# Optimization experiments

Hardware: AMD Instinct MI355X
Metric: run time of the kernel (lower is better)

The kernel has to match this reference:

```python
import jax, jax.numpy as jnp
import numpy as np

E = 512   # embed_dim == decoder_dim (structurally required by the module)
D = 512
V = 10000
B = 64
S = 32    # encoded caption length; max decode steps T = S - 1


def _lstm_cell(x, h, c, wih, whh, bih, bhh):
    # torch.nn.LSTMCell gate order: i, f, g, o
    gates = x @ wih.T + h @ whh.T + bih + bhh
    i, f, g, o = jnp.split(gates, 4, axis=-1)
    c2 = jax.nn.sigmoid(f) * c + jax.nn.sigmoid(i) * jnp.tanh(g)
    h2 = jax.nn.sigmoid(o) * jnp.tanh(c2)
    return h2, c2


def setup_inputs() -> dict:
    key = jax.random.key(0)
    ks = jax.random.split(key, 16)
    encoder_out = jax.random.normal(ks[0], (B, E), jnp.float32)
    encoded_captions = jax.random.randint(ks[1], (B, S), 0, V)
    # lengths sorted descending (required by the ragged :batch_size_t slicing); force max = S
    lens = np.sort(np.asarray(jax.random.randint(ks[2], (B,), 8, S + 1)))[::-1].copy()
    lens[0] = S
    caption_lengths = jnp.asarray(lens, jnp.int32)
    u = lambda k, sh: jax.random.uniform(k, sh, jnp.float32, -0.1, 0.1)
    return {
        'encoder_out': encoder_out,
        'encoded_captions': encoded_captions,
        'caption_lengths': caption_lengths,
        'embedding': u(ks[3], (V, E)),
        'dec_wih': u(ks[4], (4 * D, 2 * E)),
        'dec_whh': u(ks[5], (4 * D, D)),
        'dec_bih': u(ks[6], (4 * D,)),
        'dec_bhh': u(ks[7], (4 * D,)),
        'w_wih': u(ks[8], (4, E)),
        'w_whh': u(ks[9], (4, 1)),
        'w_bih': u(ks[10], (4,)),
        'w_bhh': u(ks[11], (4,)),
        'init_h_w': u(ks[12], (1, E)),
        'init_h_b': jnp.zeros((1,), jnp.float32),
        'init_c_w': u(ks[13], (1, E)),
        'init_c_b': jnp.zeros((1,), jnp.float32),
        'cls_w': u(ks[14], (V, D)),
        'cls_b': jnp.zeros((V,), jnp.float32),
    }


def reference(encoder_out, encoded_captions, caption_lengths, embedding,
              dec_wih, dec_whh, dec_bih, dec_bhh,
              w_wih, w_whh, w_bih, w_bhh,
              init_h_w, init_h_b, init_c_w, init_c_b,
              cls_w, cls_b):
    dl = caption_lengths - 1                      # decode lengths, [B]
    T = int(np.max(np.asarray(dl)))
    emb = embedding[encoded_captions]             # [B,S,E]
    xs = jnp.moveaxis(emb[:, :T, :], 1, 0)        # [T,B,E]
    wh0 = encoder_out @ init_h_w.T + init_h_b     # [B,1]
    wc0 = encoder_out @ init_c_w.T + init_c_b     # [B,1]

    def step(carry, inp):
        t, x_e = inp
        h, c, wh, wc = carry
        m = (dl > t).astype(x_e.dtype)[:, None]   # [B,1] active-row mask (ragged batch)
        wh2, wc2 = _lstm_cell(encoder_out, wh, wc, w_wih, w_whh, w_bih, w_bhh)
        x = jnp.concatenate([x_e, encoder_out], axis=-1)           # [B,2E]
        h2, c2 = _lstm_cell(x, h, c, dec_wih, dec_whh, dec_bih, dec_bhh)
        preds = (h2 @ cls_w.T + cls_b) * m        # inactive rows stay 0 (dropout is eval-mode identity)
        wgt = jax.nn.sigmoid(wh2)[:, 0] * m[:, 0] # [B]
        keep = m > 0
        carry = (jnp.where(keep, h2, h), jnp.where(keep, c2, c),
                 jnp.where(keep, wh2, wh), jnp.where(keep, wc2, wc))
        return carry, (preds, wgt)

    carry0 = (encoder_out, encoder_out, wh0, wc0)
    _, (p_seq, w_seq) = jax.lax.scan(step, carry0, (jnp.arange(T), xs))
    predictions = jnp.moveaxis(p_seq, 0, 1)                        # [B,T,V]
    weights = jnp.broadcast_to(w_seq.T[:, :, None], (B, T, V))     # replicate per-step scalar across vocab
    return predictions, dl, weights
```

## Files before the change

kernel.cpp:

```cpp
#include <hip/hip_runtime.h>
#include <hip/hip_bf16.h>


typedef __attribute__((ext_vector_type(4))) float f32x4;
typedef __attribute__((ext_vector_type(8))) short short8;
typedef __attribute__((ext_vector_type(4))) unsigned short u16x4;

#define BB 64
#define SS 32
#define TT 31
#define EE 512
#define VV 10000

__device__ __forceinline__ float sigf(float x){ return 1.0f/(1.0f + __expf(-x)); }
__device__ __forceinline__ float tanh_(float x){
  x = fminf(15.f, fmaxf(-15.f, x));
  float e = __expf(2.f*x);
  return (e-1.f)/(e+1.f);
}
__device__ __forceinline__ unsigned short f2bf(float x){
  __hip_bfloat16 h = __float2bfloat16(x);
  return __builtin_bit_cast(unsigned short, h);
}
__device__ __forceinline__ short8 cvt8(f32x4 a, f32x4 b){
  short8 t;
  t[0] = (short)f2bf(a.x); t[1] = (short)f2bf(a.y);
  t[2] = (short)f2bf(a.z); t[3] = (short)f2bf(a.w);
  t[4] = (short)f2bf(b.x); t[5] = (short)f2bf(b.y);
  t[6] = (short)f2bf(b.z); t[7] = (short)f2bf(b.w);
  return t;
}
__device__ __forceinline__ short8 ld16_coh(const void* p){
  short8 r;
  asm volatile("global_load_dwordx4 %0, %1, off sc0 sc1" : "=v"(r) : "v"(p) : "memory");
  return r;
}
__device__ __forceinline__ void st8_coh(void* p, unsigned long long v){
  asm volatile("global_store_dwordx2 %0, %1, off sc0 sc1" :: "v"(p), "v"(v) : "memory");
}

#define NPREP 2048
__global__ __launch_bounds__(256) void k_prep(
    const float* __restrict__ dwih, const float* __restrict__ dwhh,
    const float* __restrict__ emb, const int* __restrict__ cap,
    const float* __restrict__ enc,
    __hip_bfloat16* __restrict__ wihbf, __hip_bfloat16* __restrict__ whhbf,
    __hip_bfloat16* __restrict__ xa, __hip_bfloat16* __restrict__ h0,
    const int* __restrict__ caplen,
    const float* __restrict__ wwih, const float* __restrict__ wwhh,
    const float* __restrict__ wbih, const float* __restrict__ wbhh,
    const float* __restrict__ ihw, const float* __restrict__ ihb,
    const float* __restrict__ icw, const float* __restrict__ icb,
    float* __restrict__ wgt, unsigned* __restrict__ flags,
    float* __restrict__ dl_out)
{
  if (blockIdx.x >= NPREP){
    int b = blockIdx.x - NPREP;
    int w = threadIdx.x >> 6, lane = threadIdx.x & 63;
    __shared__ float sv[6];

    float p = 0.f;
    for (int k = lane; k < EE; k += 64) p += enc[b*EE + k] * wwih[w*EE + k];
    #pragma unroll
    for (int off = 32; off; off >>= 1) p += __shfl_down(p, off, 64);
    if (lane == 0) sv[w] = p;

    if (w < 2){
      const float* iw = (w == 0) ? ihw : icw;
      float q = 0.f;
      for (int k = lane; k < EE; k += 64) q += enc[b*EE + k] * iw[k];
      #pragma unroll
      for (int off = 32; off; off >>= 1) q += __shfl_down(q, off, 64);
      if (lane == 0) sv[4 + w] = q + ((w == 0) ? ihb[0] : icb[0]);
    }
    __syncthreads();

    if (threadIdx.x == 0){
      float wh = sv[4], wc = sv[5];
      int dl = caplen[b] - 1;
      for (int t = 0; t < TT; t++){
        float gi = sv[0] + wh*wwhh[0] + wbih[0] + wbhh[0];
        float gf = sv[1] + wh*wwhh[1] + wbih[1] + wbhh[1];
        float gg = sv[2] + wh*wwhh[2] + wbih[2] + wbhh[2];
        float go = sv[3] + wh*wwhh[3] + wbih[3] + wbhh[3];
        float wc2 = sigf(gf)*wc + sigf(gi)*tanh_(gg);
        float wh2 = sigf(go)*tanh_(wc2);
        float m = (dl > t) ? 1.f : 0.f;
        wgt[b*TT + t] = sigf(wh2) * m;
        if (dl > t){ wh = wh2; wc = wc2; }
      }
      dl_out[b] = (float)dl;
    }
    if (b == 0) for (int i = threadIdx.x; i < 4096; i += 256) flags[i] = 0;
    return;
  }

  const int n1 = 262144;
  const int n2 = n1 + 131072;
  const int n3 = n2 + 253952;
  const int n4 = n3 + 4096;
  for (int i = blockIdx.x*blockDim.x + threadIdx.x; i < n4; i += NPREP*256){
    const float* src; __hip_bfloat16* dst;
    if (i < n1){ src = dwih + (size_t)i*8; dst = wihbf + (size_t)i*8; }
    else if (i < n2){ int j = i - n1; src = dwhh + (size_t)j*8; dst = whhbf + (size_t)j*8; }
    else if (i < n3){
      int j = i - n2; int e = j*8;
      int r = e >> 10, k = e & 1023, t = r >> 6, b = r & 63;
      src = (k < 512) ? emb + (size_t)cap[b*SS + t]*EE + k
                      : enc + (size_t)b*EE + (k - 512);
      dst = xa + (size_t)e;
    } else {
      int j = i - n3; int e = j*8;
      src = enc + (size_t)e; dst = h0 + (size_t)e;
    }
    f32x4 lo = *(const f32x4*)src;
    f32x4 hi = *(const f32x4*)(src + 4);
    *(short8*)dst = cvt8(lo, hi);
  }
}

__global__ __launch_bounds__(256) void k_xproj(
    const __hip_bfloat16* __restrict__ xa, const __hip_bfloat16* __restrict__ wihbf,
    const float* __restrict__ bih, const float* __restrict__ bhh,
    float* __restrict__ xp)
{
  int bm = blockIdx.y;
  int bn = blockIdx.x;
  int w = threadIdx.x >> 6, lane = threadIdx.x & 63;
  int col = lane & 15, kg = lane >> 4;
  int m0 = bm*64;
  int n0 = bn*256 + w*64;

  f32x4 acc[4][4] = {};
  for (int kk = 0; kk < 32; kk++){
    short8 aW[4], aX[4];
    #pragma unroll
    for (int i = 0; i < 4; i++){
      aW[i] = *(const short8*)(wihbf + (size_t)(n0 + i*16 + col)*1024 + kk*32 + kg*8);
      aX[i] = *(const short8*)(xa    + (size_t)(m0 + i*16 + col)*1024 + kk*32 + kg*8);
    }
    #pragma unroll
    for (int nt = 0; nt < 4; nt++)
      #pragma unroll
      for (int mt = 0; mt < 4; mt++)
        acc[nt][mt] = __builtin_amdgcn_mfma_f32_16x16x32_bf16(aW[nt], aX[mt], acc[nt][mt], 0, 0, 0);
  }
  #pragma unroll
  for (int nt = 0; nt < 4; nt++){
    int n = n0 + nt*16 + 4*kg;
    f32x4 badd = *(const f32x4*)(bih + n);
    f32x4 b2   = *(const f32x4*)(bhh + n);
    badd = badd + b2;
    #pragma unroll
    for (int mt = 0; mt < 4; mt++){
      int r = m0 + mt*16 + col;
      *(f32x4*)(xp + (size_t)r*2048 + n) = acc[nt][mt] + badd;
    }
  }
}

__global__ __launch_bounds__(64, 1) void k_rec(
    const __hip_bfloat16* __restrict__ whhbf,
    const float* __restrict__ xp,
    const float* __restrict__ enc,
    const int* __restrict__ caplen,
    char* __restrict__ hbuf,
    __hip_bfloat16* __restrict__ hout,
    unsigned* __restrict__ flags,
    const float* __restrict__ clsw,
    __hip_bfloat16* __restrict__ clsbf)
{
  const int bid = blockIdx.x;
  const int lane = threadIdx.x;

  if (bid >= 128){
    const int n4 = 1280000;
    for (int i = (bid - 128)*64 + lane; i < n4; i += 384*64){
      f32x4 v = ((const f32x4*)clsw)[i];
      u16x4 o;
      o.x = f2bf(v.x); o.y = f2bf(v.y); o.z = f2bf(v.z); o.w = f2bf(v.w);
      ((u16x4*)clsbf)[i] = o;
    }
    return;
  }

  const int g = bid >> 5, s = bid & 31;
  const int col = lane & 15, kg = lane >> 4;
  const int d0 = s*16;
  const int b  = g*16 + col;
  const int dbase = d0 + 4*kg;
  const int pme = (dbase >> 2);

  short8 Aq[4][16];
  #pragma unroll
  for (int q = 0; q < 4; q++){
    const __hip_bfloat16* wrow = whhbf + (size_t)(q*512 + d0 + col)*512;
    #pragma unroll
    for (int kk = 0; kk < 16; kk++)
      Aq[q][kk] = *(const short8*)(wrow + kk*32 + kg*8);
  }
  #pragma unroll
  for (int q = 0; q < 4; q++)
    #pragma unroll
    for (int kk = 0; kk < 16; kk++)
      asm volatile("" : "+v"(Aq[q][kk]));

  float hst[4], cst[4];
  #pragma unroll
  for (int j = 0; j < 4; j++){
    float e0 = enc[(size_t)b*EE + dbase + j];
    hst[j] = e0; cst[j] = e0;
  }
  const int dl = caplen[b] - 1;
  unsigned* myflag = flags + (size_t)(g*32 + s)*32;
  const unsigned* pollflag = flags + (size_t)(g*32 + (lane & 31))*32;

  f32x4 xg[4];
  #pragma unroll
  for (int q = 0; q < 4; q++)
    xg[q] = *(const f32x4*)(xp + (size_t)b*2048 + q*512 + dbase);

  for (int t = 0; t < TT; t++){
    if (t > 0){
      const unsigned tgt = (unsigned)t;
      while (1){
        unsigned v = __hip_atomic_load(pollflag, __ATOMIC_RELAXED, __HIP_MEMORY_SCOPE_AGENT);
        v = min(v, (unsigned)__shfl_xor((int)v, 1, 64));
        v = min(v, (unsigned)__shfl_xor((int)v, 2, 64));
        v = min(v, (unsigned)__shfl_xor((int)v, 4, 64));
        v = min(v, (unsigned)__shfl_xor((int)v, 8, 64));
        v = min(v, (unsigned)__shfl_xor((int)v, 16, 64));
        if (v >= tgt) break;
        __builtin_amdgcn_s_sleep(1);
      }
    }

    const char* hc = hbuf + (size_t)(t & 1)*65536 + (size_t)b*1024 + kg*16;
    short8 Bf[16];
    #pragma unroll
    for (int kk = 0; kk < 16; kk++)
      Bf[kk] = ld16_coh(hc + kk*64);

    f32x4 xgn[4];
    if (t + 1 < TT){
      #pragma unroll
      for (int q = 0; q < 4; q++)
        xgn[q] = *(const f32x4*)(xp + (size_t)((t+1)*BB + b)*2048 + q*512 + dbase);
    }

    asm volatile("s_waitcnt vmcnt(0)" ::: "memory");
    __builtin_amdgcn_sched_barrier(0);

    f32x4 acc[4] = {};
    #pragma unroll
    for (int kk = 0; kk < 16; kk++)
      #pragma unroll
      for (int q = 0; q < 4; q++)
        acc[q] = __builtin_amdgcn_mfma_f32_16x16x32_bf16(Aq[q][kk], Bf[kk], acc[q], 0, 0, 0);

    const bool act = dl > t;
    unsigned long long hpack = 0, spack = 0;
    #pragma unroll
    for (int j = 0; j < 4; j++){
      float gi = acc[0][j] + xg[0][j];
      float gf = acc[1][j] + xg[1][j];
      float gg = acc[2][j] + xg[2][j];
      float go = acc[3][j] + xg[3][j];
      float c2 = sigf(gf)*cst[j] + sigf(gi)*tanh_(gg);
      float h2 = sigf(go)*tanh_(c2);
      if (act){ cst[j] = c2; hst[j] = h2; }
      hpack |= (unsigned long long)f2bf(h2)     << (16*j);
      spack |= (unsigned long long)f2bf(hst[j]) << (16*j);
    }

    ((unsigned long long*)hout)[((size_t)b*TT + t)*128 + pme] = hpack;

    if (t < TT - 1){
      st8_coh(hbuf + (size_t)((t + 1) & 1)*65536 + (size_t)b*1024 + (size_t)dbase*2, spack);
      asm volatile("s_waitcnt vmcnt(0)" ::: "memory");
      if (lane == 0)
        __hip_atomic_store(myflag, (unsigned)(t + 1),
                           __ATOMIC_RELAXED, __HIP_MEMORY_SCOPE_AGENT);
    }

    #pragma unroll
    for (int q = 0; q < 4; q++) xg[q] = xgn[q];
  }
}

__global__ __launch_bounds__(256) void k_cls(
    const __hip_bfloat16* __restrict__ hbf,
    const __hip_bfloat16* __restrict__ wbf,
    const float* __restrict__ clsb,
    const float* __restrict__ wgt,
    float* __restrict__ preds, float* __restrict__ wout)
{
  int bid = blockIdx.x;
  int bn = bid % 79, bm = bid / 79;
  int w = threadIdx.x >> 6, lane = threadIdx.x & 63;
  int col = lane & 15, kg = lane >> 4;
  int r0 = bm*128 + (w >> 1)*64;
  int v0 = bn*128 + (w & 1)*64;
  if (r0 >= 1984) return;

  int vrow[4], rrow[4];
  #pragma unroll
  for (int i = 0; i < 4; i++){
    vrow[i] = min(v0 + i*16 + col, VV - 1);
    rrow[i] = min(r0 + i*16 + col, 1983);
  }
  f32x4 acc[4][4] = {};
  for (int kk = 0; kk < 16; kk++){
    short8 a[4], b[4];
    #pragma unroll
    for (int i = 0; i < 4; i++){
      a[i] = *(const short8*)(wbf + (size_t)vrow[i]*512 + kk*32 + kg*8);
      b[i] = *(const short8*)(hbf + (size_t)rrow[i]*512 + kk*32 + kg*8);
    }
    #pragma unroll
    for (int vt = 0; vt < 4; vt++)
      #pragma unroll
      for (int rt = 0; rt < 4; rt++)
        acc[vt][rt] = __builtin_amdgcn_mfma_f32_16x16x32_bf16(a[vt], b[rt], acc[vt][rt], 0, 0, 0);
  }

  #pragma unroll
  for (int vt = 0; vt < 4; vt++){
    int v = v0 + vt*16 + 4*kg;
    if (v >= VV) continue;
    f32x4 cb4 = *(const f32x4*)(clsb + v);
    #pragma unroll
    for (int rt = 0; rt < 4; rt++){
      int r = r0 + rt*16 + col;
      if (r >= 1984) continue;
      float wv = wgt[r];
      float mf = (wv > 0.f) ? 1.f : 0.f;
      f32x4 o = (acc[vt][rt] + cb4) * mf;
      f32x4 wq = {wv, wv, wv, wv};
      *(f32x4*)(preds + (size_t)r*VV + v) = o;
      *(f32x4*)(wout  + (size_t)r*VV + v) = wq;
    }
  }
}

extern "C" void kernel_launch(void* const* d_in, const int* in_sizes, int n_in,
                              void* d_out, int out_size, void* d_ws, size_t ws_size,
                              hipStream_t stream) {
  const float* enc    = (const float*)d_in[0];
  const int*   cap    = (const int*)  d_in[1];
  const int*   caplen = (const int*)  d_in[2];
  const float* emb    = (const float*)d_in[3];
  const float* dwih   = (const float*)d_in[4];
  const float* dwhh   = (const float*)d_in[5];
  const float* dbih   = (const float*)d_in[6];
  const float* dbhh   = (const float*)d_in[7];
  const float* wwih   = (const float*)d_in[8];
  const float* wwhh   = (const float*)d_in[9];
  const float* wbih   = (const float*)d_in[10];
  const float* wbhh   = (const float*)d_in[11];
  const float* ihw    = (const float*)d_in[12];
  const float* ihb    = (const float*)d_in[13];
  const float* icw    = (const float*)d_in[14];
  const float* icb    = (const float*)d_in[15];
  const float* clsw   = (const float*)d_in[16];
  const float* clsb   = (const float*)d_in[17];

  float* preds  = (float*)d_out;
  float* dl_out = preds + (size_t)BB*TT*VV;
  float* wout   = dl_out + BB;

  char* ws = (char*)d_ws;
  float*          wgt   = (float*)         (ws + 0);
  unsigned*       flags = (unsigned*)      (ws + 8192);
  __hip_bfloat16* clsbf = (__hip_bfloat16*)(ws + 24576);
  __hip_bfloat16* wihbf = (__hip_bfloat16*)(ws + 10264576);
  __hip_bfloat16* whhbf = (__hip_bfloat16*)(ws + 14458880);
  __hip_bfloat16* xa    = (__hip_bfloat16*)(ws + 16556032);
  float*          xp    = (float*)         (ws + 20619264);
  char*           hbuf  = (char*)          (ws + 36872192);
  __hip_bfloat16* hout  = (__hip_bfloat16*)(ws + 37003264);

  k_prep <<<NPREP + BB, 256, 0, stream>>>(dwih, dwhh, emb, cap, enc,
                                          wihbf, whhbf, xa,
                                          (__hip_bfloat16*)hbuf,
                                          caplen, wwih, wwhh, wbih, wbhh,
                                          ihw, ihb, icw, icb, wgt, flags, dl_out);
  k_xproj<<<dim3(8, 31), 256, 0, stream>>>(xa, wihbf, dbih, dbhh, xp);
  k_rec  <<<512, 64, 0, stream>>>(whhbf, xp, enc, caplen, hbuf, hout, flags,
                                  clsw, clsbf);
  k_cls  <<<16*79, 256, 0, stream>>>(hout, clsbf, clsb, wgt, preds, wout);
}
```

Before: 292.3 us.

## Swap MFMA operand roles in classifier and split weights broadcast into separate blocks

The classifier GEMM now puts hidden rows in the A operand and vocab rows in B. Each lane therefore holds four consecutive rows for one vocab column, and lanes 0-15 write consecutive columns, so the scalar preds stores coalesce along the vocab dimension. The weights output broadcast moves out of the GEMM epilogue into 1984 extra row-blocks that stream vectorized float4 stores. This takes the strided 16-byte stores of the old layout off the GEMM tiles, at the cost of scalar 4-byte stores for preds and more blocks.

```diff
diff --git a/kernel.cpp b/kernel.cpp
--- a/kernel.cpp
+++ b/kernel.cpp
@@ -296,51 +296,65 @@
     float* __restrict__ preds, float* __restrict__ wout)
 {
   int bid = blockIdx.x;
+  if (bid >= 1264){
+    int r = bid - 1264;
+    float wv = wgt[r];
+    f32x4 wq = {wv, wv, wv, wv};
+    f32x4* dst = (f32x4*)(wout + (size_t)r*VV);
+    #pragma unroll 2
+    for (int i = threadIdx.x; i < VV/4; i += 256)
+      dst[i] = wq;
+    return;
+  }
+
   int bn = bid % 79, bm = bid / 79;
   int w = threadIdx.x >> 6, lane = threadIdx.x & 63;
   int col = lane & 15, kg = lane >> 4;
-  int r0 = bm*128 + (w >> 1)*64;
-  int v0 = bn*128 + (w & 1)*64;
-  if (r0 >= 1984) return;
-
-  int vrow[4], rrow[4];
+  int m0 = bm*128 + (w >> 1)*64;
+  int n0 = bn*128 + (w & 1)*64;
+  if (m0 >= 1984) return;
+
+  int arow[4], brow[4];
   #pragma unroll
   for (int i = 0; i < 4; i++){
-    vrow[i] = min(v0 + i*16 + col, VV - 1);
-    rrow[i] = min(r0 + i*16 + col, 1983);
+    arow[i] = min(m0 + i*16 + col, 1983);
+    brow[i] = min(n0 + i*16 + col, 9999);
   }
   f32x4 acc[4][4] = {};
   for (int kk = 0; kk < 16; kk++){
     short8 a[4], b[4];
     #pragma unroll
     for (int i = 0; i < 4; i++){
-      a[i] = *(const short8*)(wbf + (size_t)vrow[i]*512 + kk*32 + kg*8);
-      b[i] = *(const short8*)(hbf + (size_t)rrow[i]*512 + kk*32 + kg*8);
-    }
-    #pragma unroll
-    for (int vt = 0; vt < 4; vt++)
-      #pragma unroll
-      for (int rt = 0; rt < 4; rt++)
-        acc[vt][rt] = __builtin_amdgcn_mfma_f32_16x16x32_bf16(a[vt], b[rt], acc[vt][rt], 0, 0, 0);
-  }
-
-  #pragma unroll
-  for (int vt = 0; vt < 4; vt++){
-    int v = v0 + vt*16 + 4*kg;
-    if (v >= VV) continue;
-    f32x4 cb4 = *(const f32x4*)(clsb + v);
-    #pragma unroll
-    for (int rt = 0; rt < 4; rt++){
-      int r = r0 + rt*16 + col;
+      a[i] = *(const short8*)(hbf + (size_t)arow[i]*512 + kk*32 + kg*8);
+      b[i] = *(const short8*)(wbf + (size_t)brow[i]*512 + kk*32 + kg*8);
+    }
+    #pragma unroll
+    for (int mt = 0; mt < 4; mt++)
+      #pragma unroll
+      for (int nt = 0; nt < 4; nt++)
+        acc[mt][nt] = __builtin_amdgcn_mfma_f32_16x16x32_bf16(a[mt], b[nt], acc[mt][nt], 0, 0, 0);
+  }
+  float cb[4]; int vcol[4]; bool vok[4];
+  #pragma unroll
+  for (int nt = 0; nt < 4; nt++){
+    int v = n0 + nt*16 + col; vcol[nt] = v; vok[nt] = (v < VV);
+    cb[nt] = vok[nt] ? clsb[v] : 0.f;
+  }
+  #pragma unroll
+  for (int mt = 0; mt < 4; mt++)
+    #pragma unroll
+    for (int rg = 0; rg < 4; rg++){
+      int r = m0 + mt*16 + 4*kg + rg;
       if (r >= 1984) continue;
       float wv = wgt[r];
       float mf = (wv > 0.f) ? 1.f : 0.f;
-      f32x4 o = (acc[vt][rt] + cb4) * mf;
-      f32x4 wq = {wv, wv, wv, wv};
-      *(f32x4*)(preds + (size_t)r*VV + v) = o;
-      *(f32x4*)(wout  + (size_t)r*VV + v) = wq;
-    }
-  }
+      size_t base = (size_t)r*VV;
+      #pragma unroll
+      for (int nt = 0; nt < 4; nt++){
+        if (!vok[nt]) continue;
+        preds[base + vcol[nt]] = (acc[mt][nt][rg] + cb[nt]) * mf;
+      }
+    }
 }
 
 extern "C" void kernel_launch(void* const* d_in, const int* in_sizes, int n_in,
@@ -388,5 +402,5 @@
   k_xproj<<<dim3(8, 31), 256, 0, stream>>>(xa, wihbf, dbih, dbhh, xp);
   k_rec  <<<512, 64, 0, stream>>>(whhbf, xp, enc, caplen, hbuf, hout, flags,
                                   clsw, clsbf);
-  k_cls  <<<16*79, 256, 0, stream>>>(hout, clsbf, clsb, wgt, preds, wout);
-}
+  k_cls  <<<1264 + 1984, 256, 0, stream>>>(hout, clsbf, clsb, wgt, preds, wout);
+}
```

New measurement: 284.1 us. -2.8%, faster.
